# Kernel tuning notes

Hardware: AMD Instinct MI355X
Metric: run time of the kernel (lower is better)

The kernel has to match this reference:

```python
import jax, jax.numpy as jnp
import numpy as np

B, S, V, D, H, L = 2, 1024, 32000, 1024, 16, 4
DK = D // H
DF = 4 * D
EPS = 1e-5


def setup_inputs() -> dict:
    key = jax.random.key(0)
    ks = jax.random.split(key, 9)
    s = 0.02
    rn = lambda k, shape: jax.random.normal(k, shape, jnp.float32) * s
    return {
        "input_ids": jax.random.randint(ks[0], (B, S), 0, V, dtype=jnp.int32),
        "emb": rn(ks[1], (V, D)),
        "Wq": rn(ks[2], (L, D, D)),
        "Wk": rn(ks[3], (L, D, D)),
        "Wv": rn(ks[4], (L, D, D)),
        "Wo": rn(ks[5], (L, D, D)),
        "W1": rn(ks[6], (L, D, DF)),
        "b1": jnp.zeros((L, DF), jnp.float32),
        "W2": rn(ks[7], (L, DF, D)),
        "b2": jnp.zeros((L, D), jnp.float32),
        "ln1_g": jnp.ones((L, D), jnp.float32),
        "ln1_b": jnp.zeros((L, D), jnp.float32),
        "ln2_g": jnp.ones((L, D), jnp.float32),
        "ln2_b": jnp.zeros((L, D), jnp.float32),
        "lnf_g": jnp.ones((D,), jnp.float32),
        "lnf_b": jnp.zeros((D,), jnp.float32),
        "head_w": rn(ks[8], (D, V)),
    }


def _ln(x, g, b):
    m = jnp.mean(x, -1, keepdims=True)
    v = jnp.mean(jnp.square(x - m), -1, keepdims=True)
    return (x - m) * jax.lax.rsqrt(v + EPS) * g + b


def _heads(x):
    # [B,S,D] -> [B,H,S,DK]
    return x.reshape(B, S, H, DK).transpose(0, 2, 1, 3)


def _forward(input_ids, emb, Wq, Wk, Wv, Wo, W1, b1, W2, b2,
             ln1_g, ln1_b, ln2_g, ln2_b, lnf_g, lnf_b, head_w):
    x = emb[input_ids]  # [B,S,D]
    # causal mask: position q attends to k <= q (prefill, no past)
    mask = jnp.triu(jnp.full((S, S), -jnp.inf, jnp.float32), k=1)
    scale = 1.0 / np.sqrt(DK).astype(np.float32)

    def block(x, p):
        wq, wk, wv, wo, w1, bb1, w2, bb2, g1, be1, g2, be2 = p
        h = _ln(x, g1, be1)
        q = _heads(h @ wq)
        k = _heads(h @ wk)
        v = _heads(h @ wv)
        scores = jnp.einsum('bhqd,bhkd->bhqk', q, k) * scale + mask
        a = jax.nn.softmax(scores, axis=-1)
        o = jnp.einsum('bhqk,bhkd->bhqd', a, v)
        o = o.transpose(0, 2, 1, 3).reshape(B, S, D) @ wo
        x = x + o
        h2 = _ln(x, g2, be2)
        x = x + jax.nn.gelu(h2 @ w1 + bb1, approximate=False) @ w2 + bb2
        return x, None

    x, _ = jax.lax.scan(block, x, (Wq, Wk, Wv, Wo, W1, b1, W2, b2,
                                   ln1_g, ln1_b, ln2_g, ln2_b))
    logits = _ln(x, lnf_g, lnf_b) @ head_w  # [B,S,V]
    return logits


def reference(input_ids, emb, Wq, Wk, Wv, Wo, W1, b1, W2, b2,
              ln1_g, ln1_b, ln2_g, ln2_b, lnf_g, lnf_b, head_w):
    return _forward(input_ids, emb, Wq, Wk, Wv, Wo, W1, b1, W2, b2,
                    ln1_g, ln1_b, ln2_g, ln2_b, lnf_g, lnf_b, head_w)
```

## Files before the change

### kernel.cpp

```cpp
#include <hip/hip_runtime.h>
#include <stdint.h>

#define B_ 2
#define S_ 1024
#define V_ 32000
#define D_ 1024
#define H_ 16
#define L_ 4
#define DF_ 4096
#define M_ (B_*S_)

typedef short short8 __attribute__((ext_vector_type(8)));
typedef float f32x4 __attribute__((ext_vector_type(4)));

__device__ __forceinline__ unsigned short f2bf(float f){
  union { float f; unsigned int u; } v; v.f = f;
  unsigned int u = v.u;
  u = u + 0x7fffu + ((u >> 16) & 1u);
  return (unsigned short)(u >> 16);
}

__device__ __forceinline__ float bf2f(unsigned short u){
  union { unsigned int u; float f; } v; v.u = ((unsigned int)u) << 16;
  return v.f;
}

__device__ __forceinline__ void gload16(const void* g, void* l){
  __builtin_amdgcn_global_load_lds(
      (__attribute__((address_space(1))) void*)(uintptr_t)g,
      (__attribute__((address_space(3))) void*)(uintptr_t)l, 16, 0, 0);
}

__global__ __launch_bounds__(256) void embedln_k(const int* __restrict__ ids,
    const float* __restrict__ emb, const float* __restrict__ g,
    const float* __restrict__ b, float* __restrict__ x,
    unsigned short* __restrict__ out){
  int row = blockIdx.x;
  int tid = threadIdx.x;
  int id = ids[row];
  float4 v = reinterpret_cast<const float4*>(emb + (size_t)id*D_)[tid];
  reinterpret_cast<float4*>(x + (size_t)row*D_)[tid] = v;
  float s = v.x+v.y+v.z+v.w;
  float ss = v.x*v.x + v.y*v.y + v.z*v.z + v.w*v.w;
  #pragma unroll
  for (int off=1; off<64; off<<=1){ s += __shfl_xor(s, off); ss += __shfl_xor(ss, off); }
  __shared__ float rs[4], rss[4];
  int wave = tid>>6, lane = tid&63;
  if (lane==0){ rs[wave]=s; rss[wave]=ss; }
  __syncthreads();
  s  = rs[0]+rs[1]+rs[2]+rs[3];
  ss = rss[0]+rss[1]+rss[2]+rss[3];
  float mean = s * (1.0f/(float)D_);
  float var  = ss * (1.0f/(float)D_) - mean*mean;
  float inv = rsqrtf(var + 1e-5f);
  float4 gg = reinterpret_cast<const float4*>(g)[tid];
  float4 bb = reinterpret_cast<const float4*>(b)[tid];
  ushort4 o;
  o.x = f2bf((v.x-mean)*inv*gg.x + bb.x);
  o.y = f2bf((v.y-mean)*inv*gg.y + bb.y);
  o.z = f2bf((v.z-mean)*inv*gg.z + bb.z);
  o.w = f2bf((v.w-mean)*inv*gg.w + bb.w);
  reinterpret_cast<ushort4*>(out + (size_t)row*D_)[tid] = o;
}

__global__ __launch_bounds__(256) void ln_k(const float* __restrict__ x,
    const float* __restrict__ g, const float* __restrict__ b,
    unsigned short* __restrict__ out){
  int row = blockIdx.x;
  int tid = threadIdx.x;
  float4 v = reinterpret_cast<const float4*>(x + (size_t)row*D_)[tid];
  float s = v.x+v.y+v.z+v.w;
  float ss = v.x*v.x + v.y*v.y + v.z*v.z + v.w*v.w;
  #pragma unroll
  for (int off=1; off<64; off<<=1){ s += __shfl_xor(s, off); ss += __shfl_xor(ss, off); }
  __shared__ float rs[4], rss[4];
  int wave = tid>>6, lane = tid&63;
  if (lane==0){ rs[wave]=s; rss[wave]=ss; }
  __syncthreads();
  s  = rs[0]+rs[1]+rs[2]+rs[3];
  ss = rss[0]+rss[1]+rss[2]+rss[3];
  float mean = s * (1.0f/(float)D_);
  float var  = ss * (1.0f/(float)D_) - mean*mean;
  float inv = rsqrtf(var + 1e-5f);
  float4 gg = reinterpret_cast<const float4*>(g)[tid];
  float4 bb = reinterpret_cast<const float4*>(b)[tid];
  ushort4 o;
  o.x = f2bf((v.x-mean)*inv*gg.x + bb.x);
  o.y = f2bf((v.y-mean)*inv*gg.y + bb.y);
  o.z = f2bf((v.z-mean)*inv*gg.z + bb.z);
  o.w = f2bf((v.w-mean)*inv*gg.w + bb.w);
  reinterpret_cast<ushort4*>(out + (size_t)row*D_)[tid] = o;
}

__global__ __launch_bounds__(256) void rln_k(float* __restrict__ x,
    const float* __restrict__ part, const float* __restrict__ bias,
    const float* __restrict__ g, const float* __restrict__ b,
    unsigned short* __restrict__ out, int KS){
  int row = blockIdx.x;
  int tid = threadIdx.x;
  float4 v = reinterpret_cast<const float4*>(x + (size_t)row*D_)[tid];
  for (int z=0; z<KS; z++){
    float4 p = reinterpret_cast<const float4*>(part + (size_t)z*M_*D_ + (size_t)row*D_)[tid];
    v.x+=p.x; v.y+=p.y; v.z+=p.z; v.w+=p.w;
  }
  if (bias){
    float4 bb4 = reinterpret_cast<const float4*>(bias)[tid];
    v.x+=bb4.x; v.y+=bb4.y; v.z+=bb4.z; v.w+=bb4.w;
  }
  reinterpret_cast<float4*>(x + (size_t)row*D_)[tid] = v;
  float s = v.x+v.y+v.z+v.w;
  float ss = v.x*v.x + v.y*v.y + v.z*v.z + v.w*v.w;
  #pragma unroll
  for (int off=1; off<64; off<<=1){ s += __shfl_xor(s, off); ss += __shfl_xor(ss, off); }
  __shared__ float rs[4], rss[4];
  int wave = tid>>6, lane = tid&63;
  if (lane==0){ rs[wave]=s; rss[wave]=ss; }
  __syncthreads();
  s  = rs[0]+rs[1]+rs[2]+rs[3];
  ss = rss[0]+rss[1]+rss[2]+rss[3];
  float mean = s * (1.0f/(float)D_);
  float var  = ss * (1.0f/(float)D_) - mean*mean;
  float inv = rsqrtf(var + 1e-5f);
  float4 gg = reinterpret_cast<const float4*>(g)[tid];
  float4 bb = reinterpret_cast<const float4*>(b)[tid];
  ushort4 o;
  o.x = f2bf((v.x-mean)*inv*gg.x + bb.x);
  o.y = f2bf((v.y-mean)*inv*gg.y + bb.y);
  o.z = f2bf((v.z-mean)*inv*gg.z + bb.z);
  o.w = f2bf((v.w-mean)*inv*gg.w + bb.w);
  reinterpret_cast<ushort4*>(out + (size_t)row*D_)[tid] = o;
}

__global__ __launch_bounds__(256) void transpose_k(const float* __restrict__ in,
    unsigned short* __restrict__ out, int K, int N, size_t in_ls, size_t out_ls){
  __shared__ float t[64][65];
  const float* inp = in + (size_t)blockIdx.z*in_ls;
  unsigned short* outp = out + (size_t)blockIdx.z*out_ls;
  int k0 = blockIdx.y*64, n0 = blockIdx.x*64;
  int rr = threadIdx.x >> 4, c4 = (threadIdx.x & 15)*4;
  #pragma unroll
  for (int i=0;i<4;i++){
    float4 v = *reinterpret_cast<const float4*>(inp + (size_t)(k0+rr+i*16)*N + n0 + c4);
    t[rr+i*16][c4+0]=v.x; t[rr+i*16][c4+1]=v.y; t[rr+i*16][c4+2]=v.z; t[rr+i*16][c4+3]=v.w;
  }
  __syncthreads();
  const int c8 = (threadIdx.x & 7)*8;
  const int nn = threadIdx.x >> 3;
  #pragma unroll
  for (int i=0;i<2;i++){
    const int n = nn + i*32;
    unsigned short o[8];
    #pragma unroll
    for (int j=0;j<8;j++) o[j] = f2bf(t[c8+j][n]);
    *reinterpret_cast<short8*>(outp + (size_t)(n0+n)*K + k0 + c8) =
        *reinterpret_cast<const short8*>(o);
  }
}

#define VMC(n)  asm volatile("s_waitcnt vmcnt(" #n ")" ::: "memory")

#define LDA8(buf,m,ks) (*(const short8*)(lds8 + (buf)*65536 + (wm*128+(m)*16+r)*128 + (((ks)*64+g16*16)^rsw)))
#define LDB8(buf,n,ks) (*(const short8*)(lds8 + (buf)*65536 + 32768 + (wn*64+(n)*16+r)*128 + (((ks)*64+g16*16)^rsw)))
#define STG(buf,isB,h,i,tile) gload16( \
    ((isB) ? Bw + (size_t)(col0 + (h)*128 + (i)*64 + wave*8 + srow)*K + (size_t)(tile)*64 + scsw \
           : A  + (size_t)(row0 + (h)*128 + (i)*64 + wave*8 + srow)*K + (size_t)(tile)*64 + scsw), \
    lds8 + (buf)*65536 + (isB)*32768 + ((h)*128 + (i)*64 + wave*8)*128 )
#define STG_HT(buf,isB,h,tile) do{ STG(buf,isB,h,0,tile); STG(buf,isB,h,1,tile); }while(0)
#define BLOAD8(bT) do{ \
  bfr[0][0]=LDB8(bT,0,0); bfr[0][1]=LDB8(bT,0,1); bfr[1][0]=LDB8(bT,1,0); bfr[1][1]=LDB8(bT,1,1); \
  bfr[2][0]=LDB8(bT,2,0); bfr[2][1]=LDB8(bT,2,1); bfr[3][0]=LDB8(bT,3,0); bfr[3][1]=LDB8(bT,3,1); }while(0)
#define MM8(mb,n) do{ \
  acc[mb][n]    =__builtin_amdgcn_mfma_f32_16x16x32_bf16(a0[0],bfr[n][0],acc[mb][n],0,0,0); \
  acc[mb][n]    =__builtin_amdgcn_mfma_f32_16x16x32_bf16(a0[1],bfr[n][1],acc[mb][n],0,0,0); \
  acc[(mb)+1][n]=__builtin_amdgcn_mfma_f32_16x16x32_bf16(a1[0],bfr[n][0],acc[(mb)+1][n],0,0,0); \
  acc[(mb)+1][n]=__builtin_amdgcn_mfma_f32_16x16x32_bf16(a1[1],bfr[n][1],acc[(mb)+1][n],0,0,0); }while(0)
#define PH8(bT, mb, STAGES, TAIL) do{ \
  short8 a0[2], a1[2]; \
  a0[0]=LDA8(bT,mb,0); a0[1]=LDA8(bT,mb,1); a1[0]=LDA8(bT,(mb)+1,0); a1[1]=LDA8(bT,(mb)+1,1); \
  STAGES; \
  __builtin_amdgcn_s_barrier(); \
  asm volatile("s_waitcnt lgkmcnt(0)" ::: "memory"); \
  __builtin_amdgcn_s_setprio(1); \
  MM8(mb,0); MM8(mb,1); MM8(mb,2); MM8(mb,3); \
  __builtin_amdgcn_s_setprio(0); \
  TAIL; \
  __builtin_amdgcn_s_barrier(); \
}while(0)

__global__ __launch_bounds__(512, 2)
void gemm_8ph(const unsigned short* __restrict__ A, const unsigned short* __restrict__ Bw,
              float* __restrict__ C, int K, int ldc, int MB){
  __shared__ char lds8[131072];
  const int tid = threadIdx.x;
  const int wave = tid>>6, lane = tid&63;
  const int wm = wave>>2, wn = wave&3;
  const int nwg = gridDim.x;
  const int pp = blockIdx.x;
  const int t = (nwg & 7) ? pp : ((pp & 7)*(nwg>>3) + (pp>>3));
  const int by = t % MB, bx = t / MB;
  const int row0 = by*256, col0 = bx*256;
  const int r = lane&15, g16 = lane>>4;
  const int rsw = (r&7)<<4;
  const int srow = lane>>3;
  const int scsw = ((lane&7) ^ srow)*8;

  f32x4 acc[8][4] = {};
  short8 bfr[4][2];
  const int NT = K/64;

  STG_HT(0,1,0,0); STG_HT(0,1,1,0);
  STG_HT(0,0,0,0); STG_HT(0,0,1,0);
  STG_HT(1,1,0,1); STG_HT(1,1,1,1);
  VMC(4);
  __builtin_amdgcn_s_barrier();

  for (int T0 = 0; T0 < NT-2; T0 += 2){
    BLOAD8(0);
    PH8(0, 0, STG_HT(1,0,0,T0+1), ((void)0));
    PH8(0, 2, STG_HT(1,0,1,T0+1), ((void)0));
    PH8(0, 4, STG_HT(0,1,0,T0+2), ((void)0));
    PH8(0, 6, STG_HT(0,1,1,T0+2), VMC(4));
    BLOAD8(1);
    PH8(1, 0, STG_HT(0,0,0,T0+2), ((void)0));
    PH8(1, 2, STG_HT(0,0,1,T0+2), ((void)0));
    PH8(1, 4, STG_HT(1,1,0,T0+3), ((void)0));
    PH8(1, 6, STG_HT(1,1,1,T0+3), VMC(4));
  }
  BLOAD8(0);
  PH8(0, 0, STG_HT(1,0,0,NT-1), ((void)0));
  PH8(0, 2, STG_HT(1,0,1,NT-1), ((void)0));
  PH8(0, 4, ((void)0), ((void)0));
  PH8(0, 6, ((void)0), VMC(0));
  BLOAD8(1);
  PH8(1, 0, ((void)0), ((void)0));
  PH8(1, 2, ((void)0), ((void)0));
  PH8(1, 4, ((void)0), ((void)0));
  PH8(1, 6, ((void)0), ((void)0));

  #pragma unroll
  for (int m=0;m<8;m++){
    const int row = row0 + wm*128 + m*16 + g16*4;
    #pragma unroll
    for (int n=0;n<4;n++){
      const int col = col0 + wn*64 + n*16 + r;
      #pragma unroll
      for (int j=0;j<4;j++)
        C[(size_t)(row+j)*ldc + col] = acc[m][n][j];
    }
  }
}

#define L4A(buf,m,ks) (*(const short8*)(lds4 + (buf)*49152 + (wm*64+(m)*16+r)*128 + (((ks)*64+g16*16)^rsw)))
#define L4B(buf,n,ks) (*(const short8*)(lds4 + (buf)*49152 + 16384 + (wn*64+(n)*16+r)*128 + (((ks)*64+g16*16)^rsw)))
#define STG4A(buf,tile) do{ \
  gload16(A4 + (size_t)(row0 + 0*64 + wave*8 + srow)*K + (size_t)(tile)*64 + scsw, lds4 + (buf)*49152 + (0*64+wave*8)*128); \
  gload16(A4 + (size_t)(row0 + 1*64 + wave*8 + srow)*K + (size_t)(tile)*64 + scsw, lds4 + (buf)*49152 + (1*64+wave*8)*128); }while(0)
#define STG4B(buf,tile) do{ \
  gload16(B4 + (size_t)(col0 + 0*64 + wave*8 + srow)*K + (size_t)(tile)*64 + scsw, lds4 + (buf)*49152 + 16384 + (0*64+wave*8)*128); \
  gload16(B4 + (size_t)(col0 + 1*64 + wave*8 + srow)*K + (size_t)(tile)*64 + scsw, lds4 + (buf)*49152 + 16384 + (1*64+wave*8)*128); \
  gload16(B4 + (size_t)(col0 + 2*64 + wave*8 + srow)*K + (size_t)(tile)*64 + scsw, lds4 + (buf)*49152 + 16384 + (2*64+wave*8)*128); \
  gload16(B4 + (size_t)(col0 + 3*64 + wave*8 + srow)*K + (size_t)(tile)*64 + scsw, lds4 + (buf)*49152 + 16384 + (3*64+wave*8)*128); }while(0)
#define BLOAD4(bT) do{ \
  bfr4[0][0]=L4B(bT,0,0); bfr4[0][1]=L4B(bT,0,1); bfr4[1][0]=L4B(bT,1,0); bfr4[1][1]=L4B(bT,1,1); \
  bfr4[2][0]=L4B(bT,2,0); bfr4[2][1]=L4B(bT,2,1); bfr4[3][0]=L4B(bT,3,0); bfr4[3][1]=L4B(bT,3,1); }while(0)
#define MM44(mb,n) do{ \
  acc[mb][n]    =__builtin_amdgcn_mfma_f32_16x16x32_bf16(a0[0],bfr4[n][0],acc[mb][n],0,0,0); \
  acc[mb][n]    =__builtin_amdgcn_mfma_f32_16x16x32_bf16(a0[1],bfr4[n][1],acc[mb][n],0,0,0); \
  acc[(mb)+1][n]=__builtin_amdgcn_mfma_f32_16x16x32_bf16(a1[0],bfr4[n][0],acc[(mb)+1][n],0,0,0); \
  acc[(mb)+1][n]=__builtin_amdgcn_mfma_f32_16x16x32_bf16(a1[1],bfr4[n][1],acc[(mb)+1][n],0,0,0); }while(0)
#define PH4(bT, mb, STAGES, TAIL) do{ \
  short8 a0[2], a1[2]; \
  a0[0]=L4A(bT,mb,0); a0[1]=L4A(bT,mb,1); a1[0]=L4A(bT,(mb)+1,0); a1[1]=L4A(bT,(mb)+1,1); \
  STAGES; \
  __builtin_amdgcn_s_barrier(); \
  asm volatile("s_waitcnt lgkmcnt(0)" ::: "memory"); \
  __builtin_amdgcn_s_setprio(1); \
  MM44(mb,0); MM44(mb,1); MM44(mb,2); MM44(mb,3); \
  __builtin_amdgcn_s_setprio(0); \
  TAIL; \
  __builtin_amdgcn_s_barrier(); \
}while(0)

template<int EP>
__global__ __launch_bounds__(512, 2)
void gemm_4ph(const unsigned short* __restrict__ A, const unsigned short* __restrict__ Bw,
              void* __restrict__ C, const float* __restrict__ bias,
              int K, int ldc, int MB, int kLen){
  __shared__ char lds4[98304];
  const int tid = threadIdx.x;
  const int wave = tid>>6, lane = tid&63;
  const int wm = wave>>2, wn = wave&3;
  const int nwg = gridDim.x;
  const int pp = blockIdx.x;
  const int t = (nwg & 7) ? pp : ((pp & 7)*(nwg>>3) + (pp>>3));
  const int by = t % MB, bx = t / MB;
  const int row0 = by*128, col0 = bx*256;
  const int r = lane&15, g16 = lane>>4;
  const int rsw = (r&7)<<4;
  const int srow = lane>>3;
  const int scsw = ((lane&7) ^ srow)*8;
  const int kz = blockIdx.z;
  const unsigned short* A4 = A + (size_t)kz*kLen;
  const unsigned short* B4 = Bw + (size_t)kz*kLen;

  f32x4 acc[4][4] = {};
  short8 bfr4[4][2];
  const int NT = kLen/64;

  STG4B(0,0); STG4A(0,0); STG4B(1,1);
  VMC(4);
  __builtin_amdgcn_s_barrier();

  for (int T0 = 0; T0 < NT-2; T0 += 2){
    BLOAD4(0);
    PH4(0, 0, STG4A(1,T0+1), ((void)0));
    PH4(0, 2, STG4B(0,T0+2), VMC(4));
    BLOAD4(1);
    PH4(1, 0, STG4A(0,T0+2), ((void)0));
    PH4(1, 2, STG4B(1,T0+3), VMC(4));
  }
  BLOAD4(0);
  PH4(0, 0, STG4A(1,NT-1), ((void)0));
  PH4(0, 2, ((void)0), VMC(0));
  BLOAD4(1);
  PH4(1, 0, ((void)0), ((void)0));
  PH4(1, 2, ((void)0), ((void)0));

  float* Cp5 = (float*)C + (size_t)kz*M_*ldc;
  #pragma unroll
  for (int m=0;m<4;m++){
    const int row = row0 + wm*64 + m*16 + g16*4;
    #pragma unroll
    for (int n=0;n<4;n++){
      const int col = col0 + wn*64 + n*16 + r;
      #pragma unroll
      for (int j=0;j<4;j++){
        float val = acc[m][n][j];
        size_t idx = (size_t)(row+j)*ldc + col;
        if constexpr (EP==2) { val += bias[col]; val = 0.5f*val*(1.0f + erff(val*0.70710678118f)); }
        if constexpr (EP==0 || EP==2) ((unsigned short*)C)[idx] = f2bf(val);
        else Cp5[idx] = val;
      }
    }
  }
}

__global__ __launch_bounds__(256)
void attn_k(const unsigned short* __restrict__ qkv, unsigned short* __restrict__ o){
  __shared__ unsigned short Ks[2][64*64];
  __shared__ unsigned short Vt[2][64*64];
  __shared__ unsigned short Ps[4*16*64];
  const int tid = threadIdx.x;
  const int wave = tid>>6, lane = tid&63;
  const int qb = blockIdx.x, h = blockIdx.y, b = blockIdx.z;
  const int r = lane&15, g = lane>>4;
  const size_t rowbase = (size_t)b*S_*3*D_;
  const unsigned short* kbase = qkv + rowbase + D_ + h*64;
  const unsigned short* vbase = qkv + rowbase + 2*D_ + h*64;
  short8 qf[2];
  {
    const unsigned short* qp = qkv + rowbase + (size_t)(qb*64 + wave*16 + r)*(3*D_) + h*64 + g*8;
    short8 q0 = *reinterpret_cast<const short8*>(qp);
    short8 q1 = *reinterpret_cast<const short8*>(qp + 32);
    #pragma unroll
    for (int j=0;j<8;j++){
      qf[0][j] = (short)f2bf(bf2f((unsigned short)q0[j])*0.125f);
      qf[1][j] = (short)f2bf(bf2f((unsigned short)q1[j])*0.125f);
    }
  }
  float mrow[4] = {-INFINITY,-INFINITY,-INFINITY,-INFINITY};
  float lrow[4] = {0.f,0.f,0.f,0.f};
  f32x4 oacc[4] = {};
  const int qglob0 = qb*64 + wave*16 + g*4;
  unsigned short* Pw = Ps + wave*16*64;
  uint4 vdr[2];

  const int key8 = tid>>3;
  const int c8   = (tid&7)*8;
  const int kcsw = ((tid&7) ^ (key8&7))*16;

#define KSTG_A(nxt, kt2) do{ \
  gload16((const char*)(kbase + (size_t)((kt2)*64+key8)*(3*D_)) + kcsw, (char*)Ks[nxt] + wave*1024); \
  gload16((const char*)(kbase + (size_t)((kt2)*64+32+key8)*(3*D_)) + kcsw, (char*)Ks[nxt] + 4096 + wave*1024); \
}while(0)
#define VLOAD_A(kt2) do{ \
  vdr[0] = *reinterpret_cast<const uint4*>(vbase + (size_t)((kt2)*64+key8)*(3*D_) + c8); \
  vdr[1] = *reinterpret_cast<const uint4*>(vbase + (size_t)((kt2)*64+32+key8)*(3*D_) + c8); \
}while(0)
#define VSTORE_A(nxt) do{ \
  _Pragma("unroll") \
  for (int i=0;i<2;i++){ \
    int key = i*32 + key8; \
    const unsigned short* ve = reinterpret_cast<const unsigned short*>(&vdr[i]); \
    _Pragma("unroll") \
    for (int j=0;j<8;j++){ \
      int d = c8 + j; \
      int bo2 = (d*128 + key*2) ^ ((d&7)<<4); \
      *reinterpret_cast<unsigned short*>((char*)Vt[nxt] + bo2) = ve[j]; \
    } \
  } }while(0)

  KSTG_A(0, 0);
  VLOAD_A(0);
  VMC(0);
  VSTORE_A(0);
  __syncthreads();

  int cur = 0;
  for (int kt=0; kt<=qb; kt++){
    const bool pf = (kt < qb);
    if (pf){ KSTG_A(cur^1, kt+1); VLOAD_A(kt+1); }
    f32x4 sacc[4] = {};
    #pragma unroll
    for (int ks=0; ks<2; ks++){
      #pragma unroll
      for (int nb=0; nb<4; nb++){
        int key = nb*16 + r;
        int bo = (key*128 + (ks*32+g*8)*2) ^ ((key&7)<<4);
        short8 kf = *reinterpret_cast<const short8*>((char*)Ks[cur] + bo);
        sacc[nb] = __builtin_amdgcn_mfma_f32_16x16x32_bf16(qf[ks], kf, sacc[nb], 0,0,0);
      }
    }
    float sv[4][4];
    float tm[4] = {-INFINITY,-INFINITY,-INFINITY,-INFINITY};
    if (kt == qb){
      #pragma unroll
      for (int nb=0; nb<4; nb++){
        int key = kt*64 + nb*16 + r;
        #pragma unroll
        for (int j=0;j<4;j++){
          float s = (key <= qglob0 + j) ? sacc[nb][j] : -INFINITY;
          sv[nb][j] = s;
          tm[j] = fmaxf(tm[j], s);
        }
      }
    } else {
      #pragma unroll
      for (int nb=0; nb<4; nb++)
        #pragma unroll
        for (int j=0;j<4;j++){
          float s = sacc[nb][j];
          sv[nb][j] = s;
          tm[j] = fmaxf(tm[j], s);
        }
    }
    #pragma unroll
    for (int off=1; off<16; off<<=1){
      #pragma unroll
      for (int j=0;j<4;j++) tm[j] = fmaxf(tm[j], __shfl_xor(tm[j], off));
    }
    int chg = 0;
    float mn[4];
    #pragma unroll
    for (int j=0;j<4;j++){ mn[j] = fmaxf(mrow[j], tm[j]); chg |= (mn[j] > mrow[j]); }
    if (__any(chg)){
      #pragma unroll
      for (int j=0;j<4;j++){
        float sf = __expf(mrow[j]-mn[j]);
        mrow[j] = mn[j];
        lrow[j] *= sf;
        #pragma unroll
        for (int nb=0;nb<4;nb++) oacc[nb][j] *= sf;
      }
    }
    float psum[4] = {0.f,0.f,0.f,0.f};
    #pragma unroll
    for (int nb=0; nb<4; nb++){
      #pragma unroll
      for (int j=0;j<4;j++){
        float p = __expf(sv[nb][j]-mrow[j]);
        psum[j] += p;
        int prow = g*4+j;
        int bo = (prow*128 + (nb*16+r)*2) ^ ((prow&7)<<4);
        *reinterpret_cast<unsigned short*>((char*)Pw + bo) = f2bf(p);
      }
    }
    #pragma unroll
    for (int off=1; off<16; off<<=1){
      #pragma unroll
      for (int j=0;j<4;j++) psum[j] += __shfl_xor(psum[j], off);
    }
    #pragma unroll
    for (int j=0;j<4;j++) lrow[j] += psum[j];
    asm volatile("s_waitcnt lgkmcnt(0)" ::: "memory");
    #pragma unroll
    for (int ks=0; ks<2; ks++){
      int bo = (r*128 + (ks*32+g*8)*2) ^ ((r&7)<<4);
      short8 pf8 = *reinterpret_cast<const short8*>((char*)Pw + bo);
      #pragma unroll
      for (int nb=0; nb<4; nb++){
        int d = nb*16 + r;
        int bo2 = (d*128 + (ks*32+g*8)*2) ^ ((d&7)<<4);
        short8 vf = *reinterpret_cast<const short8*>((char*)Vt[cur] + bo2);
        oacc[nb] = __builtin_amdgcn_mfma_f32_16x16x32_bf16(pf8, vf, oacc[nb], 0,0,0);
      }
    }
    if (pf){ VMC(0); VSTORE_A(cur^1); }
    __syncthreads();
    cur ^= 1;
  }
  #pragma unroll
  for (int nb=0; nb<4; nb++){
    #pragma unroll
    for (int j=0;j<4;j++){
      float ov = oacc[nb][j] / lrow[j];
      size_t row = (size_t)b*S_ + qb*64 + wave*16 + g*4 + j;
      o[row*D_ + h*64 + nb*16 + r] = f2bf(ov);
    }
  }
}

extern "C" void kernel_launch(void* const* d_in, const int* in_sizes, int n_in,
                              void* d_out, int out_size, void* d_ws, size_t ws_size,
                              hipStream_t stream) {
  const int*   ids   = (const int*)  d_in[0];
  const float* emb   = (const float*)d_in[1];
  const float* Wq    = (const float*)d_in[2];
  const float* Wk    = (const float*)d_in[3];
  const float* Wv    = (const float*)d_in[4];
  const float* Wo    = (const float*)d_in[5];
  const float* W1    = (const float*)d_in[6];
  const float* b1    = (const float*)d_in[7];
  const float* W2    = (const float*)d_in[8];
  const float* b2    = (const float*)d_in[9];
  const float* ln1_g = (const float*)d_in[10];
  const float* ln1_b = (const float*)d_in[11];
  const float* ln2_g = (const float*)d_in[12];
  const float* ln2_b = (const float*)d_in[13];
  const float* lnf_g = (const float*)d_in[14];
  const float* lnf_b = (const float*)d_in[15];
  const float* headw = (const float*)d_in[16];

  unsigned short* ws = (unsigned short*)d_ws;
  unsigned short* wqkvT = ws;
  unsigned short* woT   = wqkvT + (size_t)L_*3*D_*D_;
  unsigned short* w1T   = woT   + (size_t)L_*D_*D_;
  unsigned short* w2T   = w1T   + (size_t)L_*D_*DF_;
  unsigned short* headT = w2T   + (size_t)L_*D_*DF_;
  unsigned short* h     = headT + (size_t)V_*D_;
  unsigned short* qkv   = h     + (size_t)M_*D_;
  unsigned short* attno = qkv   + (size_t)M_*3*D_;
  unsigned short* h2    = attno + (size_t)M_*D_;
  float*          x     = (float*)(h2 + (size_t)M_*DF_);
  float*          part  = x + (size_t)M_*D_;
  size_t needed = ((char*)(part + (size_t)4*M_*D_)) - (char*)d_ws;
  const bool splitk = (ws_size >= needed);

  transpose_k<<<dim3(D_/64, D_/64, L_), 256, 0, stream>>>(Wq, wqkvT,            D_, D_, (size_t)D_*D_, (size_t)3*D_*D_);
  transpose_k<<<dim3(D_/64, D_/64, L_), 256, 0, stream>>>(Wk, wqkvT + D_*D_,    D_, D_, (size_t)D_*D_, (size_t)3*D_*D_);
  transpose_k<<<dim3(D_/64, D_/64, L_), 256, 0, stream>>>(Wv, wqkvT + 2*D_*D_,  D_, D_, (size_t)D_*D_, (size_t)3*D_*D_);
  transpose_k<<<dim3(D_/64, D_/64, L_), 256, 0, stream>>>(Wo, woT,              D_, D_, (size_t)D_*D_, (size_t)D_*D_);
  transpose_k<<<dim3(DF_/64, D_/64, L_), 256, 0, stream>>>(W1, w1T,             D_, DF_, (size_t)D_*DF_, (size_t)D_*DF_);
  transpose_k<<<dim3(D_/64, DF_/64, L_), 256, 0, stream>>>(W2, w2T,             DF_, D_, (size_t)D_*DF_, (size_t)D_*DF_);
  transpose_k<<<dim3(V_/64, D_/64, 1), 256, 0, stream>>>(headw, headT,          D_, V_, 0, 0);

  embedln_k<<<M_, 256, 0, stream>>>(ids, emb, ln1_g, ln1_b, x, h);

  for (int l = 0; l < L_; l++){
    gemm_4ph<0><<<dim3((3*D_/256)*(M_/128), 1, 1), 512, 0, stream>>>(h, wqkvT + (size_t)l*3*D_*D_, qkv, nullptr, D_, 3*D_, M_/128, D_);
    attn_k<<<dim3(S_/64, H_, B_), 256, 0, stream>>>(qkv, attno);
    gemm_4ph<5><<<dim3((D_/256)*(M_/128), 1, 4), 512, 0, stream>>>(attno, woT + (size_t)l*D_*D_, part, nullptr, D_, D_, M_/128, D_/4);
    rln_k<<<M_, 256, 0, stream>>>(x, part, nullptr, ln2_g + l*D_, ln2_b + l*D_, h, 4);
    gemm_4ph<2><<<dim3((DF_/256)*(M_/128), 1, 1), 512, 0, stream>>>(h, w1T + (size_t)l*D_*DF_, h2, b1 + l*DF_, D_, DF_, M_/128, D_);
    const float* ng = (l+1 < L_) ? (ln1_g + (l+1)*D_) : lnf_g;
    const float* nb = (l+1 < L_) ? (ln1_b + (l+1)*D_) : lnf_b;
    gemm_4ph<5><<<dim3((D_/256)*(M_/128), 1, 4), 512, 0, stream>>>(h2, w2T + (size_t)l*D_*DF_, part, nullptr, DF_, D_, M_/128, DF_/4);
    rln_k<<<M_, 256, 0, stream>>>(x, part, b2 + l*D_, ng, nb, h, 4);
  }

  gemm_8ph<<<dim3((V_/256)*(M_/256), 1, 1), 512, 0, stream>>>(h, headT, (float*)d_out, D_, V_, M_/256);
}
```

Baseline: 888.9 us.

## Process two key blocks per attention iteration instead of double-buffered prefetch

The flash-attention loop now loads two 64-key K/V blocks per iteration into both LDS buffers, computes QK^T for both, applies a single online-softmax update across 128 keys, and runs PV on both. This halves the number of barrier and rescale steps and the max/sum shuffle reductions per key. In exchange it drops the overlap of next-block global loads with current compute, so load latency is exposed at the start of each iteration, and register and LDS use grow. The unused split-k workspace check is also removed.

Measured after the change: 861.1 us. -3.1%, faster.

```diff
diff --git a/kernel.cpp b/kernel.cpp
--- a/kernel.cpp
+++ b/kernel.cpp
@@ -349,7 +349,7 @@
 void attn_k(const unsigned short* __restrict__ qkv, unsigned short* __restrict__ o){
   __shared__ unsigned short Ks[2][64*64];
   __shared__ unsigned short Vt[2][64*64];
-  __shared__ unsigned short Ps[4*16*64];
+  __shared__ unsigned short Ps[2][4*16*64];
   const int tid = threadIdx.x;
   const int wave = tid>>6, lane = tid&63;
   const int qb = blockIdx.x, h = blockIdx.y, b = blockIdx.z;
@@ -372,66 +372,83 @@
   float lrow[4] = {0.f,0.f,0.f,0.f};
   f32x4 oacc[4] = {};
   const int qglob0 = qb*64 + wave*16 + g*4;
-  unsigned short* Pw = Ps + wave*16*64;
-  uint4 vdr[2];
+  unsigned short* Pw0 = Ps[0] + wave*16*64;
+  unsigned short* Pw1 = Ps[1] + wave*16*64;
+  uint4 vd0[2], vd1[2];
 
   const int key8 = tid>>3;
   const int c8   = (tid&7)*8;
   const int kcsw = ((tid&7) ^ (key8&7))*16;
 
-#define KSTG_A(nxt, kt2) do{ \
-  gload16((const char*)(kbase + (size_t)((kt2)*64+key8)*(3*D_)) + kcsw, (char*)Ks[nxt] + wave*1024); \
-  gload16((const char*)(kbase + (size_t)((kt2)*64+32+key8)*(3*D_)) + kcsw, (char*)Ks[nxt] + 4096 + wave*1024); \
+#define KSTG2(i, hb) do{ \
+  gload16((const char*)(kbase + (size_t)((hb)*64+key8)*(3*D_)) + kcsw, (char*)Ks[i] + wave*1024); \
+  gload16((const char*)(kbase + (size_t)((hb)*64+32+key8)*(3*D_)) + kcsw, (char*)Ks[i] + 4096 + wave*1024); \
 }while(0)
-#define VLOAD_A(kt2) do{ \
-  vdr[0] = *reinterpret_cast<const uint4*>(vbase + (size_t)((kt2)*64+key8)*(3*D_) + c8); \
-  vdr[1] = *reinterpret_cast<const uint4*>(vbase + (size_t)((kt2)*64+32+key8)*(3*D_) + c8); \
+#define VLOAD2(vd, hb) do{ \
+  vd[0] = *reinterpret_cast<const uint4*>(vbase + (size_t)((hb)*64+key8)*(3*D_) + c8); \
+  vd[1] = *reinterpret_cast<const uint4*>(vbase + (size_t)((hb)*64+32+key8)*(3*D_) + c8); \
 }while(0)
-#define VSTORE_A(nxt) do{ \
+#define VSTORE2(i, vd) do{ \
   _Pragma("unroll") \
-  for (int i=0;i<2;i++){ \
-    int key = i*32 + key8; \
-    const unsigned short* ve = reinterpret_cast<const unsigned short*>(&vdr[i]); \
+  for (int ii=0;ii<2;ii++){ \
+    int key = ii*32 + key8; \
+    const unsigned short* ve = reinterpret_cast<const unsigned short*>(&vd[ii]); \
     _Pragma("unroll") \
     for (int j=0;j<8;j++){ \
       int d = c8 + j; \
       int bo2 = (d*128 + key*2) ^ ((d&7)<<4); \
-      *reinterpret_cast<unsigned short*>((char*)Vt[nxt] + bo2) = ve[j]; \
+      *reinterpret_cast<unsigned short*>((char*)Vt[i] + bo2) = ve[j]; \
     } \
   } }while(0)
-
-  KSTG_A(0, 0);
-  VLOAD_A(0);
-  VMC(0);
-  VSTORE_A(0);
-  __syncthreads();
-
-  int cur = 0;
-  for (int kt=0; kt<=qb; kt++){
-    const bool pf = (kt < qb);
-    if (pf){ KSTG_A(cur^1, kt+1); VLOAD_A(kt+1); }
-    f32x4 sacc[4] = {};
-    #pragma unroll
-    for (int ks=0; ks<2; ks++){
+#define QKT2(sacc, i) do{ \
+  _Pragma("unroll") \
+  for (int ks=0; ks<2; ks++){ \
+    _Pragma("unroll") \
+    for (int nb=0; nb<4; nb++){ \
+      int key = nb*16 + r; \
+      int bo = (key*128 + (ks*32+g*8)*2) ^ ((key&7)<<4); \
+      short8 kf = *reinterpret_cast<const short8*>((char*)Ks[i] + bo); \
+      sacc[nb] = __builtin_amdgcn_mfma_f32_16x16x32_bf16(qf[ks], kf, sacc[nb], 0,0,0); \
+    } \
+  } }while(0)
+#define PV2(i, PwX) do{ \
+  _Pragma("unroll") \
+  for (int ks=0; ks<2; ks++){ \
+    int bo = (r*128 + (ks*32+g*8)*2) ^ ((r&7)<<4); \
+    short8 pf8 = *reinterpret_cast<const short8*>((char*)(PwX) + bo); \
+    _Pragma("unroll") \
+    for (int nb=0; nb<4; nb++){ \
+      int d = nb*16 + r; \
+      int bo2 = (d*128 + (ks*32+g*8)*2) ^ ((d&7)<<4); \
+      short8 vf = *reinterpret_cast<const short8*>((char*)Vt[i] + bo2); \
+      oacc[nb] = __builtin_amdgcn_mfma_f32_16x16x32_bf16(pf8, vf, oacc[nb], 0,0,0); \
+    } \
+  } }while(0)
+
+  for (int t = 0; 2*t <= qb; ++t){
+    const int hb0 = 2*t;
+    const bool v1 = (hb0 + 1 <= qb);
+    KSTG2(0, hb0);
+    if (v1) KSTG2(1, hb0+1);
+    VLOAD2(vd0, hb0);
+    if (v1) VLOAD2(vd1, hb0+1);
+    VMC(0);
+    VSTORE2(0, vd0);
+    if (v1) VSTORE2(1, vd1);
+    __syncthreads();
+    f32x4 sacc0[4] = {}, sacc1[4] = {};
+    QKT2(sacc0, 0);
+    if (v1) QKT2(sacc1, 1);
+    float sv0[4][4], sv1[4][4];
+    float tm[4] = {-INFINITY,-INFINITY,-INFINITY,-INFINITY};
+    if (hb0 == qb){
       #pragma unroll
       for (int nb=0; nb<4; nb++){
-        int key = nb*16 + r;
-        int bo = (key*128 + (ks*32+g*8)*2) ^ ((key&7)<<4);
-        short8 kf = *reinterpret_cast<const short8*>((char*)Ks[cur] + bo);
-        sacc[nb] = __builtin_amdgcn_mfma_f32_16x16x32_bf16(qf[ks], kf, sacc[nb], 0,0,0);
-      }
-    }
-    float sv[4][4];
-    float tm[4] = {-INFINITY,-INFINITY,-INFINITY,-INFINITY};
-    if (kt == qb){
-      #pragma unroll
-      for (int nb=0; nb<4; nb++){
-        int key = kt*64 + nb*16 + r;
+        int key = hb0*64 + nb*16 + r;
         #pragma unroll
         for (int j=0;j<4;j++){
-          float s = (key <= qglob0 + j) ? sacc[nb][j] : -INFINITY;
-          sv[nb][j] = s;
-          tm[j] = fmaxf(tm[j], s);
+          float s = (key <= qglob0 + j) ? sacc0[nb][j] : -INFINITY;
+          sv0[nb][j] = s; tm[j] = fmaxf(tm[j], s);
         }
       }
     } else {
@@ -439,10 +456,30 @@
       for (int nb=0; nb<4; nb++)
         #pragma unroll
         for (int j=0;j<4;j++){
-          float s = sacc[nb][j];
-          sv[nb][j] = s;
-          tm[j] = fmaxf(tm[j], s);
+          float s = sacc0[nb][j];
+          sv0[nb][j] = s; tm[j] = fmaxf(tm[j], s);
         }
+    }
+    if (v1){
+      if (hb0 + 1 == qb){
+        #pragma unroll
+        for (int nb=0; nb<4; nb++){
+          int key = (hb0+1)*64 + nb*16 + r;
+          #pragma unroll
+          for (int j=0;j<4;j++){
+            float s = (key <= qglob0 + j) ? sacc1[nb][j] : -INFINITY;
+            sv1[nb][j] = s; tm[j] = fmaxf(tm[j], s);
+          }
+        }
+      } else {
+        #pragma unroll
+        for (int nb=0; nb<4; nb++)
+          #pragma unroll
+          for (int j=0;j<4;j++){
+            float s = sacc1[nb][j];
+            sv1[nb][j] = s; tm[j] = fmaxf(tm[j], s);
+          }
+      }
     }
     #pragma unroll
     for (int off=1; off<16; off<<=1){
@@ -468,11 +505,24 @@
     for (int nb=0; nb<4; nb++){
       #pragma unroll
       for (int j=0;j<4;j++){
-        float p = __expf(sv[nb][j]-mrow[j]);
+        float p = __expf(sv0[nb][j]-mrow[j]);
         psum[j] += p;
         int prow = g*4+j;
         int bo = (prow*128 + (nb*16+r)*2) ^ ((prow&7)<<4);
-        *reinterpret_cast<unsigned short*>((char*)Pw + bo) = f2bf(p);
+        *reinterpret_cast<unsigned short*>((char*)Pw0 + bo) = f2bf(p);
+      }
+    }
+    if (v1){
+      #pragma unroll
+      for (int nb=0; nb<4; nb++){
+        #pragma unroll
+        for (int j=0;j<4;j++){
+          float p = __expf(sv1[nb][j]-mrow[j]);
+          psum[j] += p;
+          int prow = g*4+j;
+          int bo = (prow*128 + (nb*16+r)*2) ^ ((prow&7)<<4);
+          *reinterpret_cast<unsigned short*>((char*)Pw1 + bo) = f2bf(p);
+        }
       }
     }
     #pragma unroll
@@ -483,21 +533,9 @@
     #pragma unroll
     for (int j=0;j<4;j++) lrow[j] += psum[j];
     asm volatile("s_waitcnt lgkmcnt(0)" ::: "memory");
-    #pragma unroll
-    for (int ks=0; ks<2; ks++){
-      int bo = (r*128 + (ks*32+g*8)*2) ^ ((r&7)<<4);
-      short8 pf8 = *reinterpret_cast<const short8*>((char*)Pw + bo);
-      #pragma unroll
-      for (int nb=0; nb<4; nb++){
-        int d = nb*16 + r;
-        int bo2 = (d*128 + (ks*32+g*8)*2) ^ ((d&7)<<4);
-        short8 vf = *reinterpret_cast<const short8*>((char*)Vt[cur] + bo2);
-        oacc[nb] = __builtin_amdgcn_mfma_f32_16x16x32_bf16(pf8, vf, oacc[nb], 0,0,0);
-      }
-    }
-    if (pf){ VMC(0); VSTORE_A(cur^1); }
+    PV2(0, Pw0);
+    if (v1) PV2(1, Pw1);
     __syncthreads();
-    cur ^= 1;
   }
   #pragma unroll
   for (int nb=0; nb<4; nb++){
@@ -543,8 +581,6 @@
   unsigned short* h2    = attno + (size_t)M_*D_;
   float*          x     = (float*)(h2 + (size_t)M_*DF_);
   float*          part  = x + (size_t)M_*D_;
-  size_t needed = ((char*)(part + (size_t)4*M_*D_)) - (char*)d_ws;
-  const bool splitk = (ws_size >= needed);
 
   transpose_k<<<dim3(D_/64, D_/64, L_), 256, 0, stream>>>(Wq, wqkvT,            D_, D_, (size_t)D_*D_, (size_t)3*D_*D_);
   transpose_k<<<dim3(D_/64, D_/64, L_), 256, 0, stream>>>(Wk, wqkvT + D_*D_,    D_, D_, (size_t)D_*D_, (size_t)3*D_*D_);
```
